# Optimization experiments

Measured on AMD Instinct MI355X. Metric: run time of the kernel, lower is better.

## Reference

```python
import jax, jax.numpy as jnp
import numpy as np

NUM_RAYS = 131072
NUM_EXISTING = 256
NUM_SAMPLES = 96
NEAR, FAR = 2.0, 6.0


def setup_inputs() -> dict:
    key = jax.random.key(0)
    k_w, = jax.random.split(key, 1)
    weights = jax.random.uniform(k_w, (NUM_RAYS, NUM_EXISTING, 1), dtype=jnp.float32)
    # existing bins: uniform partition of [0,1] in normalized spacing coordinates
    edges = jnp.linspace(0.0, 1.0, NUM_EXISTING + 1, dtype=jnp.float32)
    spacing_starts = jnp.broadcast_to(edges[:-1, None], (NUM_RAYS, NUM_EXISTING, 1))
    spacing_ends = jnp.broadcast_to(edges[1:, None], (NUM_RAYS, NUM_EXISTING, 1))
    return {
        "weights": weights,
        "spacing_starts": spacing_starts,
        "spacing_ends": spacing_ends,
        "num_samples": NUM_SAMPLES,
    }


def _pdf_sample(weights, spacing_starts, spacing_ends, num_samples, eps=1e-5):
    num_bins = num_samples + 1  # static Python int
    w = weights[..., 0]                                   # [R, N]
    w_sum = jnp.sum(w, axis=-1, keepdims=True)            # [R, 1]
    padding = jax.nn.relu(eps - w_sum)
    w = w + padding / w.shape[-1]
    w_sum = w_sum + padding
    pdf = w / w_sum
    cdf = jnp.minimum(jnp.ones_like(pdf), jnp.cumsum(pdf, axis=-1))
    cdf = jnp.concatenate([jnp.zeros_like(cdf[..., :1]), cdf], axis=-1)  # [R, N+1]

    # eval path: deterministic bin midpoints in CDF space
    u = jnp.linspace(0.0, 1.0 - 1.0 / num_bins, num_bins, dtype=cdf.dtype)
    u = u + 1.0 / (2 * num_bins)
    u = jnp.broadcast_to(u, (*cdf.shape[:-1], num_bins))   # [R, num_bins]

    existing_bins = jnp.concatenate(
        [spacing_starts[..., 0], spacing_ends[..., -1:, 0]], axis=-1
    )                                                       # [R, N+1]

    # per-ray binary search (right bisection), vmapped over rays
    inds = jax.vmap(lambda c, uu: jnp.searchsorted(c, uu, side="right"))(cdf, u)
    last = existing_bins.shape[-1] - 1
    below = jnp.clip(inds - 1, 0, last)
    above = jnp.clip(inds, 0, last)

    cdf_g0 = jnp.take_along_axis(cdf, below, axis=-1)
    bins_g0 = jnp.take_along_axis(existing_bins, below, axis=-1)
    cdf_g1 = jnp.take_along_axis(cdf, above, axis=-1)
    bins_g1 = jnp.take_along_axis(existing_bins, above, axis=-1)

    denom = cdf_g1 - cdf_g0
    denom = jnp.where(denom < 1e-5, jnp.ones_like(denom), denom)
    t = jnp.clip((u - cdf_g0) / denom, 0.0, 1.0)
    bins = bins_g0 + t * (bins_g1 - bins_g0)
    bins = jax.lax.stop_gradient(bins)  # .detach() in original

    euclidean_bins = NEAR + bins * (FAR - NEAR)  # spacing_to_euclidean_fn (linear)
    # stack [euclidean_bins, spacing_bins]: [2, R, num_bins]
    return jnp.stack([euclidean_bins, bins], axis=0)


def reference(weights, spacing_starts, spacing_ends, num_samples):
    return _pdf_sample(weights, spacing_starts, spacing_ends, num_samples)
```

## Files before the change

kernel.cpp:

```cpp
#include <hip/hip_runtime.h>


#define NUM_RAYS 131072
#define NUM_EXISTING 256
#define NUM_BINS 97
#define EPS_W 1e-5f

constexpr int WAVES_PER_BLOCK = 4;
constexpr int BLOCK = 64 * WAVES_PER_BLOCK;
constexpr int ROW  = NUM_EXISTING + 4;
constexpr int CROW = NUM_EXISTING + 4;
constexpr int HROW = 128;

__global__ __launch_bounds__(BLOCK) void pdf_sample_kernel(
    const float* __restrict__ weights,
    const float* __restrict__ spacing_starts,
    const float* __restrict__ spacing_ends,
    float* __restrict__ out)
{
    __shared__ __align__(16) float s_bin[WAVES_PER_BLOCK][ROW];
    __shared__ __align__(16) float s_cdf[WAVES_PER_BLOCK][CROW];
    __shared__ __align__(16) int   s_h[WAVES_PER_BLOCK][HROW];

    const int wave = threadIdx.x >> 6;
    const int lane = threadIdx.x & 63;
    const int ray  = blockIdx.x * WAVES_PER_BLOCK + wave;

    const float* wrow = weights        + (size_t)ray * NUM_EXISTING;
    const float* srow = spacing_starts + (size_t)ray * NUM_EXISTING;

    float4 w4 = reinterpret_cast<const float4*>(wrow)[lane];
    float4 b4 = reinterpret_cast<const float4*>(srow)[lane];

    float* binw = s_bin[wave];
    float* cdfw = s_cdf[wave];
    int*   hw   = s_h[wave];

    reinterpret_cast<float4*>(binw)[lane] = b4;
    if (lane == 0)
        binw[NUM_EXISTING] = spacing_ends[(size_t)ray * NUM_EXISTING + (NUM_EXISTING - 1)];

    hw[lane]      = 0;
    hw[lane + 64] = 0;

    float sl   = (w4.x + w4.y) + (w4.z + w4.w);
    float incl = sl;
    #pragma unroll
    for (int off = 1; off < 64; off <<= 1) {
        float n = __shfl_up(incl, off);
        if (lane >= off) incl += n;
    }
    float total = __shfl(incl, 63);
    float excl  = incl - sl;

    float padding  = fmaxf(EPS_W - total, 0.0f);
    float pad_each = padding * (1.0f / (float)NUM_EXISTING);
    float inv      = 1.0f / (total + padding);

    float base = (excl + (float)(lane * 4) * pad_each) * inv;
    float cc = base + (w4.x + pad_each) * inv;  float c0 = fminf(cc, 1.0f);
    cc += (w4.y + pad_each) * inv;              float c1 = fminf(cc, 1.0f);
    cc += (w4.z + pad_each) * inv;              float c2 = fminf(cc, 1.0f);
    cc += (w4.w + pad_each) * inv;              float c3 = fminf(cc, 1.0f);

    float4 cst = make_float4(c0, c1, c2, c3);
    reinterpret_cast<float4*>(cdfw)[lane] = cst;

    #pragma unroll
    for (int k = 0; k < 4; ++k) {
        float c = (k == 0) ? c0 : (k == 1) ? c1 : (k == 2) ? c2 : c3;
        int m = (int)ceilf(fmaf(97.0f, c, -0.5f));
        m = m < 0 ? 0 : (m > 97 ? 97 : m);
        atomicAdd(&hw[m], 1);
    }

    int2 hp = *reinterpret_cast<const int2*>(&hw[2 * lane]);
    int v0 = hp.x, v1 = hp.y;
    int ps = v0 + v1;
    int pincl = ps;
    #pragma unroll
    for (int off = 1; off < 64; off <<= 1) {
        int n = __shfl_up(pincl, off);
        if (lane >= off) pincl += n;
    }
    int pexcl = pincl - ps;
    int inds0 = 1 + pexcl + v0;
    int inds1 = inds0 + v1;

    float* out_e = out + (size_t)ray * NUM_BINS;
    float* out_s = out + (size_t)NUM_RAYS * NUM_BINS + (size_t)ray * NUM_BINS;

    constexpr float U_STEP = 1.0f / (float)NUM_BINS;
    constexpr float U_HALF = 0.5f / (float)NUM_BINS;

    #pragma unroll
    for (int k = 0; k < 2; ++k) {
        int j = 2 * lane + k;
        if (j < NUM_BINS) {
            int idx   = (k == 0) ? inds0 : inds1;
            idx       = idx > 256 ? 256 : idx;
            int below = idx - 1;

            float u = fmaf((float)j, U_STEP, U_HALF);

            int cb = below - 1; cb = cb < 0 ? 0 : cb;
            float x = cdfw[cb];
            float y = cdfw[cb + 1];
            float cg0 = (below == 0) ? 0.0f : x;
            float cg1 = (below == 0) ? x    : y;

            float bg0 = binw[below];
            float bg1 = binw[below + 1];

            float denom = cg1 - cg0;
            denom = (denom < 1e-5f) ? 1.0f : denom;
            float t = __fdividef(u - cg0, denom);
            t = fminf(fmaxf(t, 0.0f), 1.0f);

            float bins = fmaf(t, bg1 - bg0, bg0);

            out_e[j] = fmaf(bins, 4.0f, 2.0f);
            out_s[j] = bins;
        }
    }
}

extern "C" void kernel_launch(void* const* d_in, const int* in_sizes, int n_in,
                              void* d_out, int out_size, void* d_ws, size_t ws_size,
                              hipStream_t stream) {
    const float* weights        = (const float*)d_in[0];
    const float* spacing_starts = (const float*)d_in[1];
    const float* spacing_ends   = (const float*)d_in[2];
    float* out = (float*)d_out;

    dim3 grid(NUM_RAYS / WAVES_PER_BLOCK);
    dim3 block(BLOCK);
    pdf_sample_kernel<<<grid, block, 0, stream>>>(weights, spacing_starts, spacing_ends, out);
}
```

Baseline: 353.3 us.

## Replace histogram atomics and shuffle scans with DPP scan and direct index fill

The wave-level prefix sum over the weights now uses DPP row-shift and row-broadcast adds plus a readlane instead of a shuffle-based scan loop. The LDS atomic histogram and its second prefix scan are removed. Each lane instead writes the below-index directly for the range of sample slots its four CDF entries cover, using a neighbour's bin boundary. Divisions become hardware reciprocals, which trades exact IEEE rounding for fewer instructions; the main cost is still global memory traffic.

```diff
diff --git a/kernel.cpp b/kernel.cpp
--- a/kernel.cpp
+++ b/kernel.cpp
@@ -9,8 +9,14 @@
 constexpr int WAVES_PER_BLOCK = 4;
 constexpr int BLOCK = 64 * WAVES_PER_BLOCK;
 constexpr int ROW  = NUM_EXISTING + 4;
-constexpr int CROW = NUM_EXISTING + 4;
-constexpr int HROW = 128;
+constexpr int CROW = NUM_EXISTING;
+constexpr int DROW = 128;
+
+template<int CTRL, int RMASK>
+__device__ __forceinline__ float scan_add(float v) {
+    int t = __builtin_amdgcn_update_dpp(0, __float_as_int(v), CTRL, RMASK, 0xF, true);
+    return v + __int_as_float(t);
+}
 
 __global__ __launch_bounds__(BLOCK) void pdf_sample_kernel(
     const float* __restrict__ weights,
@@ -20,7 +26,7 @@
 {
     __shared__ __align__(16) float s_bin[WAVES_PER_BLOCK][ROW];
     __shared__ __align__(16) float s_cdf[WAVES_PER_BLOCK][CROW];
-    __shared__ __align__(16) int   s_h[WAVES_PER_BLOCK][HROW];
+    __shared__ __align__(16) int   s_dn[WAVES_PER_BLOCK][DROW];
 
     const int wave = threadIdx.x >> 6;
     const int lane = threadIdx.x & 63;
@@ -34,58 +40,60 @@
 
     float* binw = s_bin[wave];
     float* cdfw = s_cdf[wave];
-    int*   hw   = s_h[wave];
+    int*   dnw  = s_dn[wave];
 
     reinterpret_cast<float4*>(binw)[lane] = b4;
     if (lane == 0)
-        binw[NUM_EXISTING] = spacing_ends[(size_t)ray * NUM_EXISTING + (NUM_EXISTING - 1)];
+        binw[NUM_EXISTING] = spacing_ends[(size_t)ray * NUM_EXISTING + NUM_EXISTING - 1];
 
-    hw[lane]      = 0;
-    hw[lane + 64] = 0;
+    dnw[lane]      = 0;
+    dnw[lane + 64] = 0;
 
-    float sl   = (w4.x + w4.y) + (w4.z + w4.w);
-    float incl = sl;
-    #pragma unroll
-    for (int off = 1; off < 64; off <<= 1) {
-        float n = __shfl_up(incl, off);
-        if (lane >= off) incl += n;
-    }
-    float total = __shfl(incl, 63);
+    float sl = (w4.x + w4.y) + (w4.z + w4.w);
+    float v = sl;
+    v = scan_add<0x111, 0xF>(v);
+    v = scan_add<0x112, 0xF>(v);
+    v = scan_add<0x114, 0xF>(v);
+    v = scan_add<0x118, 0xF>(v);
+    v = scan_add<0x142, 0xA>(v);
+    v = scan_add<0x143, 0xC>(v);
+    float incl  = v;
+    float total = __int_as_float(__builtin_amdgcn_readlane(__float_as_int(v), 63));
     float excl  = incl - sl;
 
-    float padding  = fmaxf(EPS_W - total, 0.0f);
-    float pad_each = padding * (1.0f / (float)NUM_EXISTING);
-    float inv      = 1.0f / (total + padding);
+    float padding = fmaxf(EPS_W - total, 0.0f);
+    float inv     = __builtin_amdgcn_rcpf(total + padding);
+    float padinv  = padding * inv * (1.0f / (float)NUM_EXISTING);
 
-    float base = (excl + (float)(lane * 4) * pad_each) * inv;
-    float cc = base + (w4.x + pad_each) * inv;  float c0 = fminf(cc, 1.0f);
-    cc += (w4.y + pad_each) * inv;              float c1 = fminf(cc, 1.0f);
-    cc += (w4.z + pad_each) * inv;              float c2 = fminf(cc, 1.0f);
-    cc += (w4.w + pad_each) * inv;              float c3 = fminf(cc, 1.0f);
+    float base = fmaf(excl, inv, (float)(4 * lane) * padinv);
+    float cc = base;
+    cc = fmaf(w4.x, inv, cc + padinv); float c0 = fminf(cc, 1.0f);
+    cc = fmaf(w4.y, inv, cc + padinv); float c1 = fminf(cc, 1.0f);
+    cc = fmaf(w4.z, inv, cc + padinv); float c2 = fminf(cc, 1.0f);
+    cc = fmaf(w4.w, inv, cc + padinv); float c3 = fminf(cc, 1.0f);
 
-    float4 cst = make_float4(c0, c1, c2, c3);
-    reinterpret_cast<float4*>(cdfw)[lane] = cst;
+    reinterpret_cast<float4*>(cdfw)[lane] = make_float4(c0, c1, c2, c3);
 
-    #pragma unroll
-    for (int k = 0; k < 4; ++k) {
-        float c = (k == 0) ? c0 : (k == 1) ? c1 : (k == 2) ? c2 : c3;
-        int m = (int)ceilf(fmaf(97.0f, c, -0.5f));
-        m = m < 0 ? 0 : (m > 97 ? 97 : m);
-        atomicAdd(&hw[m], 1);
-    }
+    int m0 = (int)ceilf(fmaf(97.0f, c0, -0.5f));
+    int m1 = (int)ceilf(fmaf(97.0f, c1, -0.5f));
+    int m2 = (int)ceilf(fmaf(97.0f, c2, -0.5f));
+    int m3 = (int)ceilf(fmaf(97.0f, c3, -0.5f));
 
-    int2 hp = *reinterpret_cast<const int2*>(&hw[2 * lane]);
-    int v0 = hp.x, v1 = hp.y;
-    int ps = v0 + v1;
-    int pincl = ps;
-    #pragma unroll
-    for (int off = 1; off < 64; off <<= 1) {
-        int n = __shfl_up(pincl, off);
-        if (lane >= off) pincl += n;
-    }
-    int pexcl = pincl - ps;
-    int inds0 = 1 + pexcl + v0;
-    int inds1 = inds0 + v1;
+    int mn = __shfl_down(m0, 1);
+    mn = (lane == 63) ? NUM_BINS : mn;
+
+    int bb3 = min(m3, mn);
+    int bb2 = min(m2, bb3);
+    int bb1 = min(m1, bb2);
+    int bb0 = min(m0, bb1);
+
+    int e1 = 4 * lane + 1;
+    for (int j = bb0; j < bb1; ++j) dnw[j] = e1;
+    for (int j = bb1; j < bb2; ++j) dnw[j] = e1 + 1;
+    for (int j = bb2; j < bb3; ++j) dnw[j] = e1 + 2;
+    for (int j = bb3; j < mn;  ++j) dnw[j] = e1 + 3;
+
+    int2 bl2 = *reinterpret_cast<const int2*>(&dnw[2 * lane]);
 
     float* out_e = out + (size_t)ray * NUM_BINS;
     float* out_s = out + (size_t)NUM_RAYS * NUM_BINS + (size_t)ray * NUM_BINS;
@@ -97,24 +105,22 @@
     for (int k = 0; k < 2; ++k) {
         int j = 2 * lane + k;
         if (j < NUM_BINS) {
-            int idx   = (k == 0) ? inds0 : inds1;
-            idx       = idx > 256 ? 256 : idx;
-            int below = idx - 1;
+            int below = k ? bl2.y : bl2.x;
+            below = below > 255 ? 255 : below;
+            int cb = below - 1; cb = cb < 0 ? 0 : cb;
 
             float u = fmaf((float)j, U_STEP, U_HALF);
 
-            int cb = below - 1; cb = cb < 0 ? 0 : cb;
-            float x = cdfw[cb];
-            float y = cdfw[cb + 1];
+            float x   = cdfw[cb];
+            float cg1 = cdfw[below];
             float cg0 = (below == 0) ? 0.0f : x;
-            float cg1 = (below == 0) ? x    : y;
 
             float bg0 = binw[below];
             float bg1 = binw[below + 1];
 
             float denom = cg1 - cg0;
             denom = (denom < 1e-5f) ? 1.0f : denom;
-            float t = __fdividef(u - cg0, denom);
+            float t = (u - cg0) * __builtin_amdgcn_rcpf(denom);
             t = fminf(fmaxf(t, 0.0f), 1.0f);
 
             float bins = fmaf(t, bg1 - bg0, bg0);
```

Measured after the change: 351.2 us. Within noise of the previous version (-0.6%).
